# Kernel tuning notes

Measured on AMD Instinct MI355X. Metric: run time of the kernel, lower is better.

## Reference

```python
import jax, jax.numpy as jnp
import numpy as np

B, T, D = 2, 2048, 1024
H = 16
HD = D // H
EPS = 1e-6


def rmsnorm(x, w):
    # x: [..., HD]
    var = jnp.mean(x * x, axis=-1, keepdims=True)
    return x * jax.lax.rsqrt(var + EPS) * w


def setup_inputs() -> dict:
    key = jax.random.key(0)
    ks = jax.random.split(key, 12)
    s = 1.0 / np.sqrt(D)
    return {
        "query": jax.random.normal(ks[0], (B, T, D), jnp.float32),
        "key_value": jax.random.normal(ks[1], (B, T, D), jnp.float32),
        "Wq": jax.random.normal(ks[2], (D, D), jnp.float32) * s,
        "bq": jnp.zeros((D,), jnp.float32),
        "Wk": jax.random.normal(ks[3], (D, D), jnp.float32) * s,
        "bk": jnp.zeros((D,), jnp.float32),
        "Wv": jax.random.normal(ks[4], (D, D), jnp.float32) * s,
        "bv": jnp.zeros((D,), jnp.float32),
        "Wo": jax.random.normal(ks[5], (D, D), jnp.float32) * s,
        "bo": jnp.zeros((D,), jnp.float32),
        "qn_w": jnp.ones((HD,), jnp.float32),
        "kn_w": jnp.ones((HD,), jnp.float32),
    }


def reference(query, key_value, Wq, bq, Wk, bk, Wv, bv, Wo, bo, qn_w, kn_w):
    scale = HD ** -0.5
    # projections -> [B, H, T, HD]
    def split_heads(x):
        return x.reshape(B, T, H, HD).transpose(0, 2, 1, 3)
    q = split_heads(query @ Wq.T + bq)
    k = split_heads(key_value @ Wk.T + bk)
    v = split_heads(key_value @ Wv.T + bv)
    q = rmsnorm(q, qn_w)
    k = rmsnorm(k, kn_w)
    attn = jnp.einsum('bhqd,bhkd->bhqk', q, k) * scale  # [B,H,T,T]
    attn = jax.nn.softmax(attn, axis=-1)
    out = jnp.einsum('bhqk,bhkd->bhqd', attn, v)
    out = out.transpose(0, 2, 1, 3).reshape(B, T, D)
    return out @ Wo.T + bo
```

## Files before the change

### kernel.cpp

```cpp
#include <hip/hip_runtime.h>
#include <stdint.h>

#define Bb 2
#define Tt 2048
#define Dd 1024
#define Hh 16
#define HDd 64
#define Mm 4096

typedef __attribute__((ext_vector_type(4))) float f32x4;
typedef __attribute__((ext_vector_type(16))) float f32x16;
typedef __attribute__((ext_vector_type(8))) __bf16 bf16x8;
typedef __attribute__((ext_vector_type(8))) short s16x8;
typedef __attribute__((ext_vector_type(4))) float fvec4;
typedef __attribute__((ext_vector_type(4))) unsigned int u32x4;

__device__ __forceinline__ float bf2f(ushort u){
  union { unsigned int i; float f; } v; v.i = ((unsigned int)u) << 16; return v.f;
}
__device__ __forceinline__ ushort f2bf(float f){
  union { float f; unsigned int i; } v; v.f = f;
  unsigned int u = v.i;
  u += 0x7FFFu + ((u >> 16) & 1u);
  return (ushort)(u >> 16);
}

__device__ __forceinline__ void gload16(const void* g, void* l){
  __builtin_amdgcn_global_load_lds(
      (const __attribute__((address_space(1))) void*)g,
      (__attribute__((address_space(3))) void*)l, 16, 0, 0);
}

__global__ __launch_bounds__(256) void cvt_all(
    const float* __restrict__ q, const float* __restrict__ kv,
    const float* __restrict__ wq, const float* __restrict__ wk,
    const float* __restrict__ wv, const float* __restrict__ wo,
    ushort* __restrict__ oq, ushort* __restrict__ okv, ushort* __restrict__ owq,
    ushort* __restrict__ owk, ushort* __restrict__ owv, ushort* __restrict__ owo)
{
  const int NQ = Mm*Dd/4;
  const int NW = Dd*Dd/4;
  int j = blockIdx.x * 256 + threadIdx.x;
  const float* s; ushort* d;
  if (j < NQ)            { s = q;  d = oq;  }
  else if ((j -= NQ) < NQ){ s = kv; d = okv; }
  else if ((j -= NQ) < NW){ s = wq; d = owq; }
  else if ((j -= NW) < NW){ s = wk; d = owk; }
  else if ((j -= NW) < NW){ s = wv; d = owv; }
  else        { j -= NW;   s = wo; d = owo; }
  fvec4 v = ((const fvec4*)s)[j];
  unsigned int lo = (unsigned int)f2bf(v.x) | ((unsigned int)f2bf(v.y) << 16);
  unsigned int hi = (unsigned int)f2bf(v.z) | ((unsigned int)f2bf(v.w) << 16);
  ((uint2*)d)[j] = make_uint2(lo, hi);
}

template<int MODE>
__device__ __forceinline__ void gemm_body(
    const ushort* __restrict__ A, const ushort* __restrict__ W,
    const float* __restrict__ bias, ushort* __restrict__ Oh, float* __restrict__ Of,
    const float* __restrict__ nw, float rmsScale,
    int m0, int n0, int N, int K)
{
  __shared__ ushort As[128*64];
  __shared__ ushort Bs[128*64];
  const int tid  = threadIdx.x;
  const int w    = tid >> 6, lid = tid & 63;
  const int lrow = lid & 15, g = lid >> 4;
  const int wm   = (w >> 1) << 6, wn = (w & 1) << 6;

  f32x4 acc[4][4] = {};

  for (int kt = 0; kt < K; kt += 64){
    __syncthreads();
    #pragma unroll
    for (int i = 0; i < 4; ++i){
      int e   = tid + i*256;
      int row = e >> 3;
      int c   = (e & 7) ^ (row & 7);
      gload16(A + (size_t)(m0 + row)*K + kt + c*8, &As[e*8]);
      gload16(W + (size_t)(n0 + row)*K + kt + c*8, &Bs[e*8]);
    }
    __syncthreads();
    #pragma unroll
    for (int kc = 0; kc < 2; ++kc){
      bf16x8 af[4], bfr[4];
      #pragma unroll
      for (int r = 0; r < 4; ++r){
        int row = wm + r*16 + lrow;
        af[r] = *(const bf16x8*)&As[row*64 + (((kc*4 + g) ^ (row & 7)) << 3)];
      }
      #pragma unroll
      for (int c = 0; c < 4; ++c){
        int row = wn + c*16 + lrow;
        bfr[c] = *(const bf16x8*)&Bs[row*64 + (((kc*4 + g) ^ (row & 7)) << 3)];
      }
      #pragma unroll
      for (int r = 0; r < 4; ++r)
        #pragma unroll
        for (int c = 0; c < 4; ++c)
          acc[r][c] = __builtin_amdgcn_mfma_f32_16x16x32_bf16(af[r], bfr[c], acc[r][c], 0, 0, 0);
    }
  }
  const int colbase = n0 + wn;
  float bv[4], wv4[4];
  #pragma unroll
  for (int c = 0; c < 4; ++c){
    bv[c] = bias[colbase + c*16 + lrow];
    if (MODE == 1) wv4[c] = nw[c*16 + lrow];
  }
  #pragma unroll
  for (int r = 0; r < 4; ++r){
    #pragma unroll
    for (int b = 0; b < 4; ++b){
      float v[4];
      #pragma unroll
      for (int c = 0; c < 4; ++c) v[c] = acc[r][c][b] + bv[c];
      float sc = 1.0f;
      if (MODE == 1){
        float ss = v[0]*v[0] + v[1]*v[1] + v[2]*v[2] + v[3]*v[3];
        ss += __shfl_xor(ss, 1, 64);
        ss += __shfl_xor(ss, 2, 64);
        ss += __shfl_xor(ss, 4, 64);
        ss += __shfl_xor(ss, 8, 64);
        sc = rsqrtf(ss * (1.0f/64.0f) + 1e-6f) * rmsScale;
      }
      int row = m0 + wm + r*16 + g*4 + b;
      #pragma unroll
      for (int c = 0; c < 4; ++c){
        int col = colbase + c*16 + lrow;
        if (MODE == 2)      Of[(size_t)row*N + col] = v[c];
        else if (MODE == 1) Oh[(size_t)row*N + col] = f2bf(v[c] * sc * wv4[c]);
        else                Oh[(size_t)row*N + col] = f2bf(v[c]);
      }
    }
  }
}

__global__ __launch_bounds__(256) void gemm_qkv(
  const ushort* __restrict__ qbf, const ushort* __restrict__ kvbf,
  const ushort* __restrict__ wq, const ushort* __restrict__ wk, const ushort* __restrict__ wv,
  const float* __restrict__ bq, const float* __restrict__ bk, const float* __restrict__ bv,
  const float* __restrict__ qnw, const float* __restrict__ knw,
  ushort* __restrict__ Q, ushort* __restrict__ Kx, ushort* __restrict__ V)
{
  int bid = (blockIdx.x & 7) * 96 + (blockIdx.x >> 3);
  int mt  = bid / 24;
  int ntg = bid % 24;
  int proj = ntg >> 3, nt = ntg & 7;
  if (proj == 0)
    gemm_body<1>(qbf, wq, bq, Q, nullptr, qnw, 0.18033688011112042f, mt*128, nt*128, Dd, Dd);
  else if (proj == 1)
    gemm_body<1>(kvbf, wk, bk, Kx, nullptr, knw, 1.0f, mt*128, nt*128, Dd, Dd);
  else
    gemm_body<0>(kvbf, wv, bv, V, nullptr, nullptr, 1.0f, mt*128, nt*128, Dd, Dd);
}

__global__ __launch_bounds__(256) void gemm_o(
  const ushort* __restrict__ X, const ushort* __restrict__ wo,
  const float* __restrict__ bo, float* __restrict__ out)
{
  int bid = (blockIdx.x & 7) * 32 + (blockIdx.x >> 3);
  int mt = bid / 8, nt = bid % 8;
  gemm_body<2>(X, wo, bo, nullptr, out, nullptr, 1.0f, mt*128, nt*128, Dd, Dd);
}

__global__ __launch_bounds__(256, 2) void attn_k(
  const ushort* __restrict__ Qb, const ushort* __restrict__ Kb,
  const ushort* __restrict__ Vb, ushort* __restrict__ Ob)
{
  __shared__ char L[65536];

  const int tid  = threadIdx.x;
  const int w    = tid >> 6, lid = tid & 63;
  const int half = w >> 1,  qw = w & 1;
  const int c31  = lid & 31, hi = lid >> 5;
  const int ti   = tid & 127;

  int bid = blockIdx.x;
  int wg  = (bid & 7) * 64 + (bid >> 3);
  int bh  = wg >> 4, qt = wg & 15;
  int bb  = bh >> 4, hh = bh & 15;
  const size_t base = (size_t)bb * Tt * Dd + (size_t)hh * HDd;

  bf16x8 qf[2][4];
  #pragma unroll
  for (int sub = 0; sub < 2; ++sub)
    #pragma unroll
    for (int kc = 0; kc < 4; ++kc)
      qf[sub][kc] = *(const bf16x8*)&Qb[base + (size_t)(qt*128 + qw*64 + sub*32 + c31)*Dd + kc*16 + hi*8];

  char* Kl = L + half*32768;
  char* Vl = Kl + 16384;

  int kfo[2][4];
  #pragma unroll
  for (int kh = 0; kh < 2; ++kh)
    #pragma unroll
    for (int kc = 0; kc < 4; ++kc)
      kfo[kh][kc] = (kh*32 + c31)*128 + (((2*kc + hi) ^ (c31 & 7)) << 4);

  int vfo[2][4];
  #pragma unroll
  for (int dh = 0; dh < 2; ++dh){
    int d = dh*32 + c31, F = ((d >> 3) ^ d) & 7;
    #pragma unroll
    for (int kcp = 0; kcp < 4; ++kcp)
      vfo[dh][kcp] = d*128 + (((2*kcp + hi) ^ F) << 4);
  }

  const int d0 = (ti & 7) * 8, key0 = (ti >> 3) * 4;
  int vso[8];
  {
    int m  = key0 >> 2;
    int c  = ((m >> 2) << 1) | (m & 1);
    int hb = ((m >> 1) & 1) * 8;
    #pragma unroll
    for (int dd = 0; dd < 8; ++dd){
      int d = d0 + dd, F = ((d >> 3) ^ d) & 7;
      vso[dd] = d*128 + ((c ^ F) << 4) + hb;
    }
  }

  const ushort* ksg[4]; char* kdst[4];
  #pragma unroll
  for (int i = 0; i < 4; ++i){
    int e = ti + i*128;
    int row = e >> 3, cc = (e & 7) ^ (row & 7);
    ksg[i]  = Kb + base + (size_t)(half*1024 + row) * Dd + cc*8;
    kdst[i] = Kl + e*16;
  }
  const ushort* vsg = Vb + base + (size_t)(half*1024 + key0) * Dd + d0;
  const size_t kstep = (size_t)64 * Dd;

  #pragma unroll
  for (int i = 0; i < 4; ++i) gload16(ksg[i], kdst[i]);
  u32x4 vv0 = *(const u32x4*)(vsg);
  u32x4 vv1 = *(const u32x4*)(vsg + Dd);
  u32x4 vv2 = *(const u32x4*)(vsg + 2*Dd);
  u32x4 vv3 = *(const u32x4*)(vsg + 3*Dd);
  #pragma unroll
  for (int i = 0; i < 4; ++i) ksg[i] += kstep;
  vsg += kstep;

  f32x16 o[2][2] = {};
  float mr[2] = {-1e30f, -1e30f};
  float lr[2] = {0.f, 0.f};

  auto vscatter = [&](int bufoff){
    #pragma unroll
    for (int dd = 0; dd < 8; ++dd){
      unsigned sel = (dd & 1) ? 0x07060302u : 0x05040100u;
      unsigned lo  = __builtin_amdgcn_perm(vv1[dd >> 1], vv0[dd >> 1], sel);
      unsigned hi2 = __builtin_amdgcn_perm(vv3[dd >> 1], vv2[dd >> 1], sel);
      *(uint2*)(Vl + vso[dd] + bufoff) = make_uint2(lo, hi2);
    }
  };

  auto dosm = [&](f32x16* s, float& m, float& l, f32x16* oo, bf16x8* pao){
    float mx = s[0][0];
    #pragma unroll
    for (int i = 1; i < 16; ++i) mx = fmaxf(mx, s[0][i]);
    #pragma unroll
    for (int i = 0; i < 16; ++i) mx = fmaxf(mx, s[1][i]);
    mx = fmaxf(mx, __shfl_xor(mx, 32, 64));
    const bool defer = (__all(mx - m <= 8.0f) != 0);
    float nm = defer ? m : fmaxf(m, mx);
    float rs = 0.f;
    #pragma unroll
    for (int kh = 0; kh < 2; ++kh)
      #pragma unroll
      for (int i = 0; i < 16; ++i){
        float e = __builtin_amdgcn_exp2f(s[kh][i] - nm);
        s[kh][i] = e; rs += e;
      }
    rs += __shfl_xor(rs, 32, 64);
    if (defer){
      l += rs;
    } else {
      float f = __builtin_amdgcn_exp2f(m - nm);
      l = l * f + rs; m = nm;
      #pragma unroll
      for (int i = 0; i < 16; ++i){ oo[0][i] *= f; oo[1][i] *= f; }
    }
    #pragma unroll
    for (int kh = 0; kh < 2; ++kh)
      #pragma unroll
      for (int c = 0; c < 2; ++c){
        unsigned u0, u1, u2, u3;
        asm("v_cvt_pk_bf16_f32 %0, %1, %2" : "=v"(u0) : "v"(s[kh][8*c+0]), "v"(s[kh][8*c+1]));
        asm("v_cvt_pk_bf16_f32 %0, %1, %2" : "=v"(u1) : "v"(s[kh][8*c+2]), "v"(s[kh][8*c+3]));
        asm("v_cvt_pk_bf16_f32 %0, %1, %2" : "=v"(u2) : "v"(s[kh][8*c+4]), "v"(s[kh][8*c+5]));
        asm("v_cvt_pk_bf16_f32 %0, %1, %2" : "=v"(u3) : "v"(s[kh][8*c+6]), "v"(s[kh][8*c+7]));
        u32x4 uu = {u0, u1, u2, u3};
        pao[kh*2 + c] = __builtin_bit_cast(bf16x8, uu);
      }
  };

#define ATTN_TILE(BUF, PREFETCH)                                                     \
  {                                                                                  \
    vscatter((BUF)*8192);                                                            \
    __syncthreads();                                                                 \
    if (PREFETCH){                                                                   \
      _Pragma("unroll")                                                              \
      for (int i = 0; i < 4; ++i){                                                   \
        gload16(ksg[i], kdst[i] + ((BUF)^1)*8192);                                   \
        ksg[i] += kstep;                                                             \
      }                                                                              \
      vv0 = *(const u32x4*)(vsg);                                                    \
      vv1 = *(const u32x4*)(vsg + Dd);                                               \
      vv2 = *(const u32x4*)(vsg + 2*Dd);                                             \
      vv3 = *(const u32x4*)(vsg + 3*Dd);                                             \
      vsg += kstep;                                                                  \
    }                                                                                \
    f32x16 s0[2] = {}, s1[2] = {};                                                   \
    __builtin_amdgcn_s_setprio(1);                                                   \
    _Pragma("unroll")                                                                \
    for (int kh = 0; kh < 2; ++kh)                                                   \
      _Pragma("unroll")                                                              \
      for (int kc = 0; kc < 4; ++kc){                                                \
        bf16x8 kf = *(const bf16x8*)(Kl + kfo[kh][kc] + (BUF)*8192);                 \
        s0[kh] = __builtin_amdgcn_mfma_f32_32x32x16_bf16(kf, qf[0][kc], s0[kh], 0,0,0); \
        s1[kh] = __builtin_amdgcn_mfma_f32_32x32x16_bf16(kf, qf[1][kc], s1[kh], 0,0,0); \
      }                                                                              \
    __builtin_amdgcn_s_setprio(0);                                                   \
    bf16x8 pa0[4], pa1[4];                                                           \
    dosm(s0, mr[0], lr[0], o[0], pa0);                                               \
    dosm(s1, mr[1], lr[1], o[1], pa1);                                               \
    __builtin_amdgcn_s_setprio(1);                                                   \
    _Pragma("unroll")                                                                \
    for (int dh = 0; dh < 2; ++dh)                                                   \
      _Pragma("unroll")                                                              \
      for (int kcp = 0; kcp < 4; ++kcp){                                             \
        bf16x8 vf = *(const bf16x8*)(Vl + vfo[dh][kcp] + (BUF)*8192);                \
        o[0][dh] = __builtin_amdgcn_mfma_f32_32x32x16_bf16(vf, pa0[kcp], o[0][dh], 0,0,0); \
        o[1][dh] = __builtin_amdgcn_mfma_f32_32x32x16_bf16(vf, pa1[kcp], o[1][dh], 0,0,0); \
      }                                                                              \
    __builtin_amdgcn_s_setprio(0);                                                   \
  }

  for (int kt2 = 0; kt2 < 8; ++kt2){
    ATTN_TILE(0, true);
    ATTN_TILE(1, (kt2 != 7));
  }
#undef ATTN_TILE

  __syncthreads();
  if (half == 1){
    #pragma unroll
    for (int sub = 0; sub < 2; ++sub)
      #pragma unroll
      for (int dh = 0; dh < 2; ++dh)
        #pragma unroll
        for (int G = 0; G < 4; ++G){
          f32x4 v = { o[sub][dh][4*G+0], o[sub][dh][4*G+1], o[sub][dh][4*G+2], o[sub][dh][4*G+3] };
          *(f32x4*)(L + (((sub*8 + dh*4 + G)*128) + ti)*16) = v;
        }
    f32x4 ml = {mr[0], lr[0], mr[1], lr[1]};
    *(f32x4*)(L + ((16*128) + ti)*16) = ml;
  }
  __syncthreads();
  if (half == 0){
    f32x4 ml = *(const f32x4*)(L + ((16*128) + ti)*16);
    #pragma unroll
    for (int sub = 0; sub < 2; ++sub){
      float ms = mr[sub], ls = lr[sub];
      float mp = ml[sub*2], lp = ml[sub*2 + 1];
      float nm = fmaxf(ms, mp);
      float es = __builtin_amdgcn_exp2f(ms - nm);
      float ep = __builtin_amdgcn_exp2f(mp - nm);
      float inv = 1.0f / (ls*es + lp*ep);
      int qrow = qt*128 + qw*64 + sub*32 + c31;
      #pragma unroll
      for (int dh = 0; dh < 2; ++dh)
        #pragma unroll
        for (int G = 0; G < 4; ++G){
          f32x4 op = *(const f32x4*)(L + (((sub*8 + dh*4 + G)*128) + ti)*16);
          float oc0 = (o[sub][dh][4*G+0]*es + op[0]*ep) * inv;
          float oc1 = (o[sub][dh][4*G+1]*es + op[1]*ep) * inv;
          float oc2 = (o[sub][dh][4*G+2]*es + op[2]*ep) * inv;
          float oc3 = (o[sub][dh][4*G+3]*es + op[3]*ep) * inv;
          uint2 u;
          u.x = (unsigned)f2bf(oc0) | ((unsigned)f2bf(oc1) << 16);
          u.y = (unsigned)f2bf(oc2) | ((unsigned)f2bf(oc3) << 16);
          *(uint2*)&Ob[base + (size_t)qrow*Dd + dh*32 + 8*G + hi*4] = u;
        }
    }
  }
}

extern "C" void kernel_launch(void* const* d_in, const int* in_sizes, int n_in,
                              void* d_out, int out_size, void* d_ws, size_t ws_size,
                              hipStream_t stream)
{
  const float* query = (const float*)d_in[0];
  const float* keyv  = (const float*)d_in[1];
  const float* Wq    = (const float*)d_in[2];
  const float* bq    = (const float*)d_in[3];
  const float* Wk    = (const float*)d_in[4];
  const float* bk    = (const float*)d_in[5];
  const float* Wv    = (const float*)d_in[6];
  const float* bv    = (const float*)d_in[7];
  const float* Wo    = (const float*)d_in[8];
  const float* bo    = (const float*)d_in[9];
  const float* qnw   = (const float*)d_in[10];
  const float* knw   = (const float*)d_in[11];
  float* out = (float*)d_out;

  char* p = (char*)d_ws;
  ushort* qbf  = (ushort*)p; p += (size_t)Mm*Dd*2;
  ushort* kvbf = (ushort*)p; p += (size_t)Mm*Dd*2;
  ushort* wqb  = (ushort*)p; p += (size_t)Dd*Dd*2;
  ushort* wkb  = (ushort*)p; p += (size_t)Dd*Dd*2;
  ushort* wvb  = (ushort*)p; p += (size_t)Dd*Dd*2;
  ushort* wob  = (ushort*)p; p += (size_t)Dd*Dd*2;
  ushort* Qb   = (ushort*)p; p += (size_t)Mm*Dd*2;
  ushort* Kbf  = (ushort*)p; p += (size_t)Mm*Dd*2;
  ushort* Vbf  = (ushort*)p; p += (size_t)Mm*Dd*2;
  ushort* Ab   = (ushort*)p; p += (size_t)Mm*Dd*2;

  cvt_all<<<dim3(12288), dim3(256), 0, stream>>>(query, keyv, Wq, Wk, Wv, Wo,
                                                 qbf, kvbf, wqb, wkb, wvb, wob);

  gemm_qkv<<<dim3(768), dim3(256), 0, stream>>>(qbf, kvbf, wqb, wkb, wvb,
                                                bq, bk, bv, qnw, knw, Qb, Kbf, Vbf);

  attn_k<<<dim3(512), dim3(256), 0, stream>>>(Qb, Kbf, Vbf, Ab);

  gemm_o<<<dim3(256), dim3(256), 0, stream>>>(Ab, wob, bo, out);
}
```

Before: 131.3 us.

## Fuse K and V projections into one block sharing the key_value A tile

Replaces the 768-block QKV GEMM grid with 512 blocks. Even blocks compute a Q tile; odd blocks compute both K and V tiles for the same rows, loading each key_value A tile once and issuing MFMAs against two weight tiles. Shared memory moves to a caller-provided 48KB buffer. The aim is to cut redundant A-tile loads and launch/tail overhead. The cost is load imbalance, since KV blocks do twice the MFMA work of Q blocks, plus doubled accumulator registers and more LDS per block, which may lower occupancy.

```diff
diff --git a/kernel.cpp b/kernel.cpp
--- a/kernel.cpp
+++ b/kernel.cpp
@@ -55,14 +55,14 @@
 }
 
 template<int MODE>
-__device__ __forceinline__ void gemm_body(
+__device__ __forceinline__ void gemm_body(char* smem,
     const ushort* __restrict__ A, const ushort* __restrict__ W,
     const float* __restrict__ bias, ushort* __restrict__ Oh, float* __restrict__ Of,
     const float* __restrict__ nw, float rmsScale,
     int m0, int n0, int N, int K)
 {
-  __shared__ ushort As[128*64];
-  __shared__ ushort Bs[128*64];
+  ushort* As = (ushort*)smem;
+  ushort* Bs = (ushort*)(smem + 16384);
   const int tid  = threadIdx.x;
   const int w    = tid >> 6, lid = tid & 63;
   const int lrow = lid & 15, g = lid >> 4;
@@ -136,32 +136,120 @@
   }
 }
 
-__global__ __launch_bounds__(256) void gemm_qkv(
+__device__ __forceinline__ void gemm_kv_body(char* smem,
+    const ushort* __restrict__ A, const ushort* __restrict__ Wk, const ushort* __restrict__ Wv,
+    const float* __restrict__ bk, const float* __restrict__ bv, const float* __restrict__ knw,
+    ushort* __restrict__ Ok, ushort* __restrict__ Ov, int m0, int n0)
+{
+  ushort* As  = (ushort*)smem;
+  ushort* Bks = (ushort*)(smem + 16384);
+  ushort* Bvs = (ushort*)(smem + 32768);
+  const int tid  = threadIdx.x;
+  const int w    = tid >> 6, lid = tid & 63;
+  const int lrow = lid & 15, g = lid >> 4;
+  const int wm   = (w >> 1) << 6, wn = (w & 1) << 6;
+
+  f32x4 ak[4][4] = {};
+  f32x4 av[4][4] = {};
+
+  for (int kt = 0; kt < Dd; kt += 64){
+    __syncthreads();
+    #pragma unroll
+    for (int i = 0; i < 4; ++i){
+      int e   = tid + i*256;
+      int row = e >> 3;
+      int c   = (e & 7) ^ (row & 7);
+      gload16(A  + (size_t)(m0 + row)*Dd + kt + c*8, &As[e*8]);
+      gload16(Wk + (size_t)(n0 + row)*Dd + kt + c*8, &Bks[e*8]);
+      gload16(Wv + (size_t)(n0 + row)*Dd + kt + c*8, &Bvs[e*8]);
+    }
+    __syncthreads();
+    #pragma unroll
+    for (int kc = 0; kc < 2; ++kc){
+      bf16x8 af[4], bk8[4], bv8[4];
+      #pragma unroll
+      for (int r = 0; r < 4; ++r){
+        int row = wm + r*16 + lrow;
+        af[r] = *(const bf16x8*)&As[row*64 + (((kc*4 + g) ^ (row & 7)) << 3)];
+      }
+      #pragma unroll
+      for (int c = 0; c < 4; ++c){
+        int row = wn + c*16 + lrow;
+        int off = row*64 + (((kc*4 + g) ^ (row & 7)) << 3);
+        bk8[c] = *(const bf16x8*)&Bks[off];
+        bv8[c] = *(const bf16x8*)&Bvs[off];
+      }
+      #pragma unroll
+      for (int r = 0; r < 4; ++r)
+        #pragma unroll
+        for (int c = 0; c < 4; ++c){
+          ak[r][c] = __builtin_amdgcn_mfma_f32_16x16x32_bf16(af[r], bk8[c], ak[r][c], 0, 0, 0);
+          av[r][c] = __builtin_amdgcn_mfma_f32_16x16x32_bf16(af[r], bv8[c], av[r][c], 0, 0, 0);
+        }
+    }
+  }
+  const int colbase = n0 + wn;
+  float bkc[4], bvc[4], wk4[4];
+  #pragma unroll
+  for (int c = 0; c < 4; ++c){
+    bkc[c] = bk[colbase + c*16 + lrow];
+    bvc[c] = bv[colbase + c*16 + lrow];
+    wk4[c] = knw[c*16 + lrow];
+  }
+  #pragma unroll
+  for (int r = 0; r < 4; ++r){
+    #pragma unroll
+    for (int b = 0; b < 4; ++b){
+      float vk[4], vv[4];
+      #pragma unroll
+      for (int c = 0; c < 4; ++c){
+        vk[c] = ak[r][c][b] + bkc[c];
+        vv[c] = av[r][c][b] + bvc[c];
+      }
+      float ss = vk[0]*vk[0] + vk[1]*vk[1] + vk[2]*vk[2] + vk[3]*vk[3];
+      ss += __shfl_xor(ss, 1, 64);
+      ss += __shfl_xor(ss, 2, 64);
+      ss += __shfl_xor(ss, 4, 64);
+      ss += __shfl_xor(ss, 8, 64);
+      float sc = rsqrtf(ss * (1.0f/64.0f) + 1e-6f);
+      int row = m0 + wm + r*16 + g*4 + b;
+      #pragma unroll
+      for (int c = 0; c < 4; ++c){
+        int col = colbase + c*16 + lrow;
+        Ok[(size_t)row*Dd + col] = f2bf(vk[c] * sc * wk4[c]);
+        Ov[(size_t)row*Dd + col] = f2bf(vv[c]);
+      }
+    }
+  }
+}
+
+__global__ __launch_bounds__(256) void gemm_qkvf(
   const ushort* __restrict__ qbf, const ushort* __restrict__ kvbf,
   const ushort* __restrict__ wq, const ushort* __restrict__ wk, const ushort* __restrict__ wv,
   const float* __restrict__ bq, const float* __restrict__ bk, const float* __restrict__ bv,
   const float* __restrict__ qnw, const float* __restrict__ knw,
   ushort* __restrict__ Q, ushort* __restrict__ Kx, ushort* __restrict__ V)
 {
-  int bid = (blockIdx.x & 7) * 96 + (blockIdx.x >> 3);
-  int mt  = bid / 24;
-  int ntg = bid % 24;
-  int proj = ntg >> 3, nt = ntg & 7;
-  if (proj == 0)
-    gemm_body<1>(qbf, wq, bq, Q, nullptr, qnw, 0.18033688011112042f, mt*128, nt*128, Dd, Dd);
-  else if (proj == 1)
-    gemm_body<1>(kvbf, wk, bk, Kx, nullptr, knw, 1.0f, mt*128, nt*128, Dd, Dd);
-  else
-    gemm_body<0>(kvbf, wv, bv, V, nullptr, nullptr, 1.0f, mt*128, nt*128, Dd, Dd);
+  __shared__ char smem[49152];
+  int wg  = (blockIdx.x & 7) * 64 + (blockIdx.x >> 3);
+  int sub = wg >> 1;
+  int mt  = sub >> 3, nt = sub & 7;
+  if ((wg & 1) == 0){
+    gemm_body<1>(smem, qbf, wq, bq, Q, nullptr, qnw, 0.18033688011112042f,
+                 mt*128, nt*128, Dd, Dd);
+  } else {
+    gemm_kv_body(smem, kvbf, wk, wv, bk, bv, knw, Kx, V, mt*128, nt*128);
+  }
 }
 
 __global__ __launch_bounds__(256) void gemm_o(
   const ushort* __restrict__ X, const ushort* __restrict__ wo,
   const float* __restrict__ bo, float* __restrict__ out)
 {
+  __shared__ char smem[32768];
   int bid = (blockIdx.x & 7) * 32 + (blockIdx.x >> 3);
   int mt = bid / 8, nt = bid % 8;
-  gemm_body<2>(X, wo, bo, nullptr, out, nullptr, 1.0f, mt*128, nt*128, Dd, Dd);
+  gemm_body<2>(smem, X, wo, bo, nullptr, out, nullptr, 1.0f, mt*128, nt*128, Dd, Dd);
 }
 
 __global__ __launch_bounds__(256, 2) void attn_k(
@@ -421,8 +509,8 @@
   cvt_all<<<dim3(12288), dim3(256), 0, stream>>>(query, keyv, Wq, Wk, Wv, Wo,
                                                  qbf, kvbf, wqb, wkb, wvb, wob);
 
-  gemm_qkv<<<dim3(768), dim3(256), 0, stream>>>(qbf, kvbf, wqb, wkb, wvb,
-                                                bq, bk, bv, qnw, knw, Qb, Kbf, Vbf);
+  gemm_qkvf<<<dim3(512), dim3(256), 0, stream>>>(qbf, kvbf, wqb, wkb, wvb,
+                                                 bq, bk, bv, qnw, knw, Qb, Kbf, Vbf);
 
   attn_k<<<dim3(512), dim3(256), 0, stream>>>(Qb, Kbf, Vbf, Ab);
 
```

Result: slower. 148.3 us (+12.9%).
